# Kernel tuning notes

Measured on AMD Instinct MI355X. Metric: run time of the kernel, lower is better.

## Reference

```python
import jax, jax.numpy as jnp
import numpy as np

N_NODES = 50000
N_EDGES = 300000
N_GRAPHS = 2048
N_FEATS = 128
DIM_OUT = 32


def setup_inputs() -> dict:
    key = jax.random.key(0)
    ks = jax.random.split(key, 10)
    def glorot(k, shape):
        fan_in, fan_out = shape
        lim = (6.0 / (fan_in + fan_out)) ** 0.5
        return jax.random.uniform(k, shape, jnp.float32, -lim, lim)
    x = jax.random.normal(ks[0], (N_NODES, N_FEATS), jnp.float32)
    edge_index = jax.random.randint(ks[1], (2, N_EDGES), 0, N_NODES, jnp.int64)
    batch = jnp.sort(jax.random.randint(ks[2], (N_NODES,), 0, N_GRAPHS, jnp.int64))
    return {
        "x": x,
        "edge_index": edge_index,
        "batch": batch,
        "W1": glorot(ks[3], (N_FEATS, 256)), "b1": jnp.zeros((256,), jnp.float32),
        "W2": glorot(ks[4], (256, 256)),     "b2": jnp.zeros((256,), jnp.float32),
        "W3": glorot(ks[5], (256, 256)),     "b3": jnp.zeros((256,), jnp.float32),
        "Wf1": glorot(ks[6], (256, 128)),    "bf1": jnp.zeros((128,), jnp.float32),
        "Wf2": glorot(ks[7], (128, DIM_OUT)), "bf2": jnp.zeros((DIM_OUT,), jnp.float32),
    }


def _gcn_norm(edge_index, num_nodes):
    # PyG GCNConv default: add self-loops, symmetric D^-1/2 (A+I) D^-1/2 norm.
    loop = jnp.arange(num_nodes, dtype=edge_index.dtype)
    src = jnp.concatenate([edge_index[0], loop])
    dst = jnp.concatenate([edge_index[1], loop])
    deg = jax.ops.segment_sum(jnp.ones_like(dst, jnp.float32), dst, num_segments=num_nodes)
    dinv = jnp.where(deg > 0, deg ** -0.5, 0.0)
    norm = dinv[src] * dinv[dst]  # [E + N]
    return src, dst, norm


def _gcn_conv(x, src, dst, norm, W, b):
    h = x @ W                                # [N, C] transform first (efficient)
    msg = h[src] * norm[:, None]             # gather + scale, [E+N, C]
    agg = jax.ops.segment_sum(msg, dst, num_segments=x.shape[0])
    return agg + b


def reference(x, edge_index, batch, W1, b1, W2, b2, W3, b3, Wf1, bf1, Wf2, bf2):
    n = x.shape[0]
    src, dst, norm = _gcn_norm(edge_index, n)
    h = jax.nn.relu(_gcn_conv(x, src, dst, norm, W1, b1))
    h = jax.nn.relu(_gcn_conv(h, src, dst, norm, W2, b2))
    h = jax.nn.relu(_gcn_conv(h, src, dst, norm, W3, b3))
    # global_mean_pool over batch segment ids
    sums = jax.ops.segment_sum(h, batch, num_segments=N_GRAPHS)
    cnts = jax.ops.segment_sum(jnp.ones((n,), jnp.float32), batch, num_segments=N_GRAPHS)
    hg = sums / jnp.maximum(cnts, 1.0)[:, None]
    h = jax.nn.relu(hg @ Wf1 + bf1)
    return h @ Wf2 + bf2  # [N_GRAPHS, DIM_OUT]
```

## Files before the change

kernel.cpp:

```cpp
#include <hip/hip_runtime.h>
#include <hip/hip_bf16.h>

#define NNODES 50000
#define NEDGES 300000
#define NGRAPH 2048
#define NFEAT  128
#define NHID   256
#define DOUT   32
#define NROWS  50048

typedef __bf16 bf16x8 __attribute__((ext_vector_type(8)));
typedef float  f32x4  __attribute__((ext_vector_type(4)));
typedef unsigned short ushort8v __attribute__((ext_vector_type(8)));
typedef __attribute__((address_space(1))) const void* gas_ptr;
typedef __attribute__((address_space(3))) void* las_ptr;

__device__ __forceinline__ float bf2f(unsigned short u) {
    return __uint_as_float(((unsigned)u) << 16);
}
__device__ __forceinline__ unsigned short f2bf(float f) {
    unsigned u = __float_as_uint(f);
    unsigned r = u + 0x7FFFu + ((u >> 16) & 1u);
    return (unsigned short)(r >> 16);
}

__global__ __launch_bounds__(256) void prep_k(const float* __restrict__ x, unsigned short* __restrict__ x16,
                                              const float* __restrict__ W1, const float* __restrict__ W2,
                                              const float* __restrict__ W3, const float* __restrict__ Wf1,
                                              const float* __restrict__ Wf2,
                                              unsigned short* __restrict__ Wt1, unsigned short* __restrict__ Wt2,
                                              unsigned short* __restrict__ Wt3, unsigned short* __restrict__ Wf1t,
                                              unsigned short* __restrict__ Wf2t,
                                              int* __restrict__ cnt, int* __restrict__ fill) {
    int idx = blockIdx.x * 256 + threadIdx.x;
    if (idx < 800000) {
        int i = idx * 8;
        float4 a = *(const float4*)&x[i];
        float4 b = *(const float4*)&x[i + 4];
        ushort4 lo = { f2bf(a.x), f2bf(a.y), f2bf(a.z), f2bf(a.w) };
        ushort4 hi = { f2bf(b.x), f2bf(b.y), f2bf(b.z), f2bf(b.w) };
        *(ushort4*)&x16[i] = lo;
        *(ushort4*)&x16[i + 4] = hi;
        return;
    }
    int t = idx - 800000;
    if (t < 200704) {
        const float* W; unsigned short* Wt; int K, N, base; bool sw;
        if      (t <  32768) { W = W1;  Wt = Wt1;  K = 128; N = 256; base = 0;      sw = true; }
        else if (t <  98304) { W = W2;  Wt = Wt2;  K = 256; N = 256; base = 32768;  sw = true; }
        else if (t < 163840) { W = W3;  Wt = Wt3;  K = 256; N = 256; base = 98304;  sw = true; }
        else if (t < 196608) { W = Wf1; Wt = Wf1t; K = 256; N = 128; base = 163840; sw = false; }
        else                 { W = Wf2; Wt = Wf2t; K = 128; N = 32;  base = 196608; sw = false; }
        int i = t - base; int n = i / K, k = i - n * K;
        unsigned short v = f2bf(W[(size_t)k * N + n]);
        if (sw) Wt[(k >> 5) * 8192 + n * 32 + (k & 31)] = v;
        else    Wt[i] = v;
        return;
    }
    t -= 200704;
    if (t < NNODES) { cnt[t] = 0; fill[t] = 0; }
}

__global__ __launch_bounds__(256) void edge_hist_k(const int* __restrict__ dst, int* cnt, int E) {
    int e = blockIdx.x * 256 + threadIdx.x;
    if (e < E) atomicAdd(&cnt[dst[e]], 1);
}

__global__ __launch_bounds__(1024) void scan_block_k(const int* __restrict__ cnt, int* __restrict__ rowp,
                                                     int* __restrict__ part, float* __restrict__ dinv, int n) {
    __shared__ int s[1024];
    int tid = threadIdx.x;
    int i = blockIdx.x * 1024 + tid;
    int v = (i < n) ? cnt[i] : 0;
    if (i < n) dinv[i] = rsqrtf((float)(v + 1));
    s[tid] = v;
    __syncthreads();
    for (int off = 1; off < 1024; off <<= 1) {
        int t = (tid >= off) ? s[tid - off] : 0;
        __syncthreads();
        s[tid] += t;
        __syncthreads();
    }
    if (i < n) rowp[i] = s[tid] - v;
    if (tid == 1023) part[blockIdx.x] = s[1023];
}

__global__ __launch_bounds__(256) void scatter_k(const int* __restrict__ src, const int* __restrict__ dst,
                                                 const int* __restrict__ rowp_pre, const int* __restrict__ part,
                                                 int* fill, const float* __restrict__ dinv,
                                                 int* __restrict__ col, float* __restrict__ nrm,
                                                 int* __restrict__ rowp_fin,
                                                 const int* __restrict__ batch, int* __restrict__ gstart,
                                                 int E, int n, int nb) {
    __shared__ int s[64];
    int tid = threadIdx.x;
    if (tid < 64) s[tid] = (tid < nb) ? part[tid] : 0;
    __syncthreads();
    for (int off = 1; off < 64; off <<= 1) {
        int t = 0;
        if (tid < 64 && tid >= off) t = s[tid - off];
        __syncthreads();
        if (tid < 64) s[tid] += t;
        __syncthreads();
    }
    int gid = blockIdx.x * 256 + tid;
    if (gid <= n) {
        if (gid < n) {
            int ch = gid >> 10;
            int base = (ch == 0) ? 0 : s[ch - 1];
            rowp_fin[gid] = rowp_pre[gid] + base;
        } else {
            rowp_fin[n] = s[nb - 1];
        }
    }
    if (gid < n) {
        int b = batch[gid];
        int prev = (gid == 0) ? -1 : batch[gid - 1];
        for (int g = prev + 1; g <= b; ++g) gstart[g] = gid;
        if (gid == n - 1)
            for (int g = b + 1; g <= NGRAPH; ++g) gstart[g] = n;
    }
    if (gid < E) {
        int ss = src[gid], d = dst[gid];
        int ch = d >> 10;
        int base = (ch == 0) ? 0 : s[ch - 1];
        int p = rowp_pre[d] + base + atomicAdd(&fill[d], 1);
        col[p] = ss;
        nrm[p] = dinv[ss] * dinv[d];
    }
}

template<int K>
__global__ __launch_bounds__(512, 2) void gemm_rs_k(const unsigned short* __restrict__ A,
                                                    const unsigned short* __restrict__ Bsw,
                                                    const float* __restrict__ bias,
                                                    unsigned short* __restrict__ C,
                                                    int M, int flags, int ntiles) {
    __shared__ unsigned short tile[2][64 * 264];
    const int tid = threadIdx.x;
    const int lane = tid & 63;
    const int wave = tid >> 6;
    const int m = lane & 15, q = lane >> 4;
    const int wr = (wave >> 2) * 32;
    const int wc = (wave & 3) * 64;

    bf16x8 breg[K / 32][4];
#pragma unroll
    for (int kt = 0; kt < K / 32; ++kt)
#pragma unroll
        for (int j = 0; j < 4; ++j)
            breg[kt][j] = *(const bf16x8*)&Bsw[kt * 8192 + (wc + j * 16 + m) * 32 + q * 8];

    int buf = 0;
    for (int t = blockIdx.x; t < ntiles; t += gridDim.x) {
        const int rowBase = t * 64;
        f32x4 acc[2][4] = {};
#pragma unroll
        for (int kt = 0; kt < K / 32; ++kt) {
            bf16x8 af[2];
#pragma unroll
            for (int i = 0; i < 2; ++i)
                af[i] = *(const bf16x8*)&A[(size_t)(rowBase + wr + i * 16 + m) * K + kt * 32 + q * 8];
#pragma unroll
            for (int i = 0; i < 2; ++i)
#pragma unroll
                for (int j = 0; j < 4; ++j)
                    acc[i][j] = __builtin_amdgcn_mfma_f32_16x16x32_bf16(af[i], breg[kt][j], acc[i][j], 0, 0, 0);
        }
        unsigned short* tb = tile[buf];
#pragma unroll
        for (int i = 0; i < 2; ++i) {
#pragma unroll
            for (int j = 0; j < 4; ++j) {
                int c = wc + j * 16 + m;
                float bv = (flags & 2) ? bias[c] : 0.f;
#pragma unroll
                for (int r = 0; r < 4; ++r) {
                    float v = acc[i][j][r] + bv;
                    if (flags & 1) v = fmaxf(v, 0.f);
                    tb[(wr + i * 16 + q * 4 + r) * 264 + c] = f2bf(v);
                }
            }
        }
        __syncthreads();
#pragma unroll
        for (int u0 = 0; u0 < 4; ++u0) {
            int u = u0 * 512 + tid;
            int row = u >> 5, cc = (u & 31) * 8;
            int rr = rowBase + row;
            if (rr < M)
                *(ushort8v*)&C[(size_t)rr * 256 + cc] = *(const ushort8v*)&tile[buf][row * 264 + cc];
        }
        buf ^= 1;
    }
}

__global__ __launch_bounds__(256) void agg128_k(const unsigned short* __restrict__ x,
                                                const int* __restrict__ rowp, const int* __restrict__ col,
                                                const float* __restrict__ nrm, const float* __restrict__ dinv,
                                                unsigned short* __restrict__ z, int n) {
    int wave = threadIdx.x >> 6;
    int lane = threadIdx.x & 63;
    int st = lane >> 4;
    int li = lane & 15;
    int node = blockIdx.x * 4 + wave;
    if (node >= n) return;
    const ushort8v* tp = (const ushort8v*)x;
    float di = dinv[node], sw = di * di;
    float hsw = (st == 0) ? sw : 0.f;
    ushort8v u = tp[(size_t)node * 16 + li];
    float ac[8];
#pragma unroll
    for (int k = 0; k < 8; ++k) ac[k] = bf2f(u[k]) * hsw;
    int e0 = rowp[node], e1 = rowp[node + 1];
    for (int e = e0 + st; e < e1; e += 8) {
        int c[2]; float w[2];
#pragma unroll
        for (int j = 0; j < 2; ++j) {
            int ee = e + 4 * j;
            bool v = ee < e1;
            c[j] = v ? col[ee] : 0;
            w[j] = v ? nrm[ee] : 0.f;
        }
        ushort8v mm[2];
#pragma unroll
        for (int j = 0; j < 2; ++j) mm[j] = tp[(size_t)c[j] * 16 + li];
#pragma unroll
        for (int j = 0; j < 2; ++j)
#pragma unroll
            for (int k = 0; k < 8; ++k)
                ac[k] += bf2f(mm[j][k]) * w[j];
    }
#pragma unroll
    for (int k = 0; k < 8; ++k) ac[k] += __shfl_down(ac[k], 32, 64);
#pragma unroll
    for (int k = 0; k < 8; ++k) ac[k] += __shfl_down(ac[k], 16, 64);
    if (st == 0) {
        ushort8v o;
#pragma unroll
        for (int k = 0; k < 8; ++k) o[k] = f2bf(ac[k]);
        ((ushort8v*)(z + (size_t)node * 128))[li] = o;
    }
}

__global__ __launch_bounds__(256) void agg256_k(const unsigned short* __restrict__ t,
                                                const int* __restrict__ rowp, const int* __restrict__ col,
                                                const float* __restrict__ nrm, const float* __restrict__ dinv,
                                                unsigned short* __restrict__ z, int n) {
    int wave = threadIdx.x >> 6;
    int lane = threadIdx.x & 63;
    int half = lane >> 5;
    int li   = lane & 31;
    int node = blockIdx.x * 4 + wave;
    if (node >= n) return;
    const ushort8v* tp = (const ushort8v*)t;
    float di = dinv[node], sw = di * di;
    float hsw = half ? 0.f : sw;
    ushort8v u = tp[(size_t)node * 32 + li];
    float ac[8];
#pragma unroll
    for (int k = 0; k < 8; ++k) ac[k] = bf2f(u[k]) * hsw;
    int e0 = rowp[node], e1 = rowp[node + 1];
    for (int e = e0 + half; e < e1; e += 8) {
        int c[4]; float w[4];
#pragma unroll
        for (int j = 0; j < 4; ++j) {
            int ee = e + 2 * j;
            bool v = ee < e1;
            c[j] = v ? col[ee] : 0;
            w[j] = v ? nrm[ee] : 0.f;
        }
        ushort8v mm[4];
#pragma unroll
        for (int j = 0; j < 4; ++j) mm[j] = tp[(size_t)c[j] * 32 + li];
#pragma unroll
        for (int j = 0; j < 4; ++j)
#pragma unroll
            for (int k = 0; k < 8; ++k)
                ac[k] += bf2f(mm[j][k]) * w[j];
    }
#pragma unroll
    for (int k = 0; k < 8; ++k) ac[k] += __shfl_down(ac[k], 32, 64);
    if (half == 0) {
        ushort8v o;
#pragma unroll
        for (int k = 0; k < 8; ++k) o[k] = f2bf(ac[k]);
        ((ushort8v*)(z + (size_t)node * NHID))[li] = o;
    }
}

__global__ __launch_bounds__(256) void pool_k(const unsigned short* __restrict__ h,
                                              const int* __restrict__ gstart,
                                              unsigned short* __restrict__ hg) {
    __shared__ float red[4][256];
    int g = blockIdx.x;
    int wave = threadIdx.x >> 6, lane = threadIdx.x & 63;
    int s = gstart[g], e = gstart[g + 1];
    const ushort4* hp = (const ushort4*)h;
    float4 acc = make_float4(0.f, 0.f, 0.f, 0.f);
    for (int i = s + wave; i < e; i += 4) {
        ushort4 v = hp[(size_t)i * 64 + lane];
        acc.x += bf2f(v.x); acc.y += bf2f(v.y); acc.z += bf2f(v.z); acc.w += bf2f(v.w);
    }
    *(float4*)&red[wave][lane * 4] = acc;
    __syncthreads();
    if (wave == 0) {
        float inv = 1.f / fmaxf((float)(e - s), 1.f);
        float v0 = red[0][lane*4+0] + red[1][lane*4+0] + red[2][lane*4+0] + red[3][lane*4+0];
        float v1 = red[0][lane*4+1] + red[1][lane*4+1] + red[2][lane*4+1] + red[3][lane*4+1];
        float v2 = red[0][lane*4+2] + red[1][lane*4+2] + red[2][lane*4+2] + red[3][lane*4+2];
        float v3 = red[0][lane*4+3] + red[1][lane*4+3] + red[2][lane*4+3] + red[3][lane*4+3];
        ushort4 o = { f2bf(v0 * inv), f2bf(v1 * inv), f2bf(v2 * inv), f2bf(v3 * inv) };
        ((ushort4*)(hg + (size_t)g * NHID))[lane] = o;
    }
}

__global__ __launch_bounds__(256) void mlp_head_k(const unsigned short* __restrict__ HG,
                                                  const unsigned short* __restrict__ Wf1t,
                                                  const unsigned short* __restrict__ Wf2t,
                                                  const float* __restrict__ bf1, const float* __restrict__ bf2,
                                                  float* __restrict__ out) {
    __shared__ unsigned short As1[128 * 32];
    __shared__ unsigned short Bs1[128 * 32];
    __shared__ unsigned short R[128 * 128];
    __shared__ unsigned short Bs2[32 * 128];
    const int tid = threadIdx.x;
    const int lane = tid & 63, wave = tid >> 6;
    const int m = lane & 15, q = lane >> 4;
    const int rowBase = blockIdx.x * 128;
    const int wr = (wave >> 1) * 64;
    const int wc = (wave & 1) * 64;

#pragma unroll
    for (int c2 = 0; c2 < 2; ++c2) {
        const unsigned short* g = &Wf2t[(c2 * 256 + tid) * 8];
        __builtin_amdgcn_global_load_lds((gas_ptr)g, (las_ptr)&Bs2[(c2 * 256 + wave * 64) * 8], 16, 0, 0);
    }

    f32x4 acc[4][4] = {};
    for (int kt = 0; kt < 256; kt += 32) {
#pragma unroll
        for (int c2 = 0; c2 < 2; ++c2) {
            int u = c2 * 256 + tid;
            int row = u >> 2, kp = u & 3;
            const unsigned short* ga = &HG[(size_t)(rowBase + row) * 256 + kt + kp * 8];
            const unsigned short* gb = &Wf1t[(size_t)row * 256 + kt + kp * 8];
            __builtin_amdgcn_global_load_lds((gas_ptr)ga, (las_ptr)&As1[(c2 * 256 + wave * 64) * 8], 16, 0, 0);
            __builtin_amdgcn_global_load_lds((gas_ptr)gb, (las_ptr)&Bs1[(c2 * 256 + wave * 64) * 8], 16, 0, 0);
        }
        __syncthreads();
        bf16x8 af[4], bfr[4];
#pragma unroll
        for (int i = 0; i < 4; ++i) af[i] = *(const bf16x8*)&As1[(wr + i * 16 + m) * 32 + q * 8];
#pragma unroll
        for (int j = 0; j < 4; ++j) bfr[j] = *(const bf16x8*)&Bs1[(wc + j * 16 + m) * 32 + q * 8];
#pragma unroll
        for (int i = 0; i < 4; ++i)
#pragma unroll
            for (int j = 0; j < 4; ++j)
                acc[i][j] = __builtin_amdgcn_mfma_f32_16x16x32_bf16(af[i], bfr[j], acc[i][j], 0, 0, 0);
        __syncthreads();
    }
#pragma unroll
    for (int i = 0; i < 4; ++i)
#pragma unroll
        for (int j = 0; j < 4; ++j) {
            int c = wc + j * 16 + m;
            float bv = bf1[c];
#pragma unroll
            for (int r = 0; r < 4; ++r) {
                int rr = wr + i * 16 + q * 4 + r;
                R[rr * 128 + c] = f2bf(fmaxf(acc[i][j][r] + bv, 0.f));
            }
        }
    __syncthreads();

    const int wr2 = wave * 32;
    f32x4 acc2[2][2] = {};
#pragma unroll
    for (int s2 = 0; s2 < 4; ++s2) {
        bf16x8 af2[2], bf22[2];
#pragma unroll
        for (int i = 0; i < 2; ++i) af2[i] = *(const bf16x8*)&R[(wr2 + i * 16 + m) * 128 + s2 * 32 + q * 8];
#pragma unroll
        for (int ct = 0; ct < 2; ++ct) bf22[ct] = *(const bf16x8*)&Bs2[(ct * 16 + m) * 128 + s2 * 32 + q * 8];
#pragma unroll
        for (int i = 0; i < 2; ++i)
#pragma unroll
            for (int ct = 0; ct < 2; ++ct)
                acc2[i][ct] = __builtin_amdgcn_mfma_f32_16x16x32_bf16(af2[i], bf22[ct], acc2[i][ct], 0, 0, 0);
    }
#pragma unroll
    for (int i = 0; i < 2; ++i)
#pragma unroll
        for (int ct = 0; ct < 2; ++ct) {
            int c = ct * 16 + m;
            float bv = bf2[c];
#pragma unroll
            for (int r = 0; r < 4; ++r) {
                int rr = rowBase + wr2 + i * 16 + q * 4 + r;
                out[(size_t)rr * 32 + c] = acc2[i][ct][r] + bv;
            }
        }
}

extern "C" void kernel_launch(void* const* d_in, const int* in_sizes, int n_in,
                              void* d_out, int out_size, void* d_ws, size_t ws_size,
                              hipStream_t stream) {
    const float* x    = (const float*)d_in[0];
    const int*   ei   = (const int*)d_in[1];
    const int*   batch= (const int*)d_in[2];
    const float* W1   = (const float*)d_in[3];
    const float* b1   = (const float*)d_in[4];
    const float* W2   = (const float*)d_in[5];
    const float* b2   = (const float*)d_in[6];
    const float* W3   = (const float*)d_in[7];
    const float* b3   = (const float*)d_in[8];
    const float* Wf1  = (const float*)d_in[9];
    const float* bf1  = (const float*)d_in[10];
    const float* Wf2  = (const float*)d_in[11];
    const float* bf2  = (const float*)d_in[12];
    float* out = (float*)d_out;

    const int* e_src = ei;
    const int* e_dst = ei + NEDGES;

    char* ws = (char*)d_ws;
    size_t off = 0;
    auto alloc = [&](size_t bytes) -> void* {
        void* p = (void*)(ws + off);
        off += (bytes + 255) & ~(size_t)255;
        return p;
    };
    unsigned short* X16 = (unsigned short*)alloc((size_t)NROWS * NFEAT * 2);
    unsigned short* Za  = (unsigned short*)alloc((size_t)NROWS * NFEAT * 2);
    unsigned short* Ha  = (unsigned short*)alloc((size_t)NROWS * NHID * 2);
    unsigned short* Zb  = (unsigned short*)alloc((size_t)NROWS * NHID * 2);
    unsigned short* Wt1 = (unsigned short*)alloc((size_t)NHID * NFEAT * 2);
    unsigned short* Wt2 = (unsigned short*)alloc((size_t)NHID * NHID * 2);
    unsigned short* Wt3 = (unsigned short*)alloc((size_t)NHID * NHID * 2);
    unsigned short* Wf1t= (unsigned short*)alloc((size_t)NFEAT * NHID * 2);
    unsigned short* Wf2t= (unsigned short*)alloc((size_t)DOUT * NFEAT * 2);
    unsigned short* HG  = (unsigned short*)alloc((size_t)NGRAPH * NHID * 2);
    float* dinv = (float*)alloc((size_t)NNODES * 4);
    int*   cnt  = (int*)alloc((size_t)NNODES * 4);
    int*   fill = (int*)alloc((size_t)NNODES * 4);
    int*   rowp = (int*)alloc((size_t)(NNODES + 1) * 4);
    int*   rowf = (int*)alloc((size_t)(NNODES + 1) * 4);
    int*   col  = (int*)alloc((size_t)NEDGES * 4);
    float* nrm  = (float*)alloc((size_t)NEDGES * 4);
    int*   part = (int*)alloc((size_t)64 * 4);
    int*   gstart = (int*)alloc((size_t)(NGRAPH + 1) * 4);
    (void)alloc(131072);

    const int nb = (NNODES + 1023) / 1024;

    hipLaunchKernelGGL(prep_k, dim3((1050704 + 255) / 256), dim3(256), 0, stream,
                       x, X16, W1, W2, W3, Wf1, Wf2, Wt1, Wt2, Wt3, Wf1t, Wf2t, cnt, fill);
    hipLaunchKernelGGL(edge_hist_k, dim3((NEDGES + 255) / 256), dim3(256), 0, stream, e_dst, cnt, NEDGES);
    hipLaunchKernelGGL(scan_block_k, dim3(nb), dim3(1024), 0, stream, cnt, rowp, part, dinv, NNODES);
    hipLaunchKernelGGL(scatter_k, dim3((NEDGES + 255) / 256), dim3(256), 0, stream,
                       e_src, e_dst, rowp, part, fill, dinv, col, nrm, rowf, batch, gstart,
                       NEDGES, NNODES, nb);

    const int ntiles = NROWS / 64;
    const int nagg  = (NNODES + 3) / 4;
    hipLaunchKernelGGL(agg128_k, dim3(nagg), dim3(256), 0, stream,
                       X16, rowf, col, nrm, dinv, Za, NNODES);
    hipLaunchKernelGGL((gemm_rs_k<128>), dim3(512), dim3(512), 0, stream,
                       Za, Wt1, b1, Ha, NNODES, 3, ntiles);
    hipLaunchKernelGGL(agg256_k, dim3(nagg), dim3(256), 0, stream,
                       Ha, rowf, col, nrm, dinv, Zb, NNODES);
    hipLaunchKernelGGL((gemm_rs_k<256>), dim3(256), dim3(512), 0, stream,
                       Zb, Wt2, b2, Ha, NNODES, 3, ntiles);
    hipLaunchKernelGGL(agg256_k, dim3(nagg), dim3(256), 0, stream,
                       Ha, rowf, col, nrm, dinv, Zb, NNODES);
    hipLaunchKernelGGL((gemm_rs_k<256>), dim3(256), dim3(512), 0, stream,
                       Zb, Wt3, b3, Ha, NNODES, 3, ntiles);

    hipLaunchKernelGGL(pool_k, dim3(NGRAPH), dim3(256), 0, stream, Ha, gstart, HG);

    hipLaunchKernelGGL(mlp_head_k, dim3(NGRAPH / 128), dim3(256), 0, stream,
                       HG, Wf1t, Wf2t, bf1, bf2, out);
}
```

Measured before the change: 301.6 us.

## Fuse neighbor aggregation into GEMM tiles and pack edge column/norm pairs

Replaces the separate aggregation kernels and row-streaming GEMMs with one fused kernel per layer. Each block gathers and normalizes the neighbor features for its 64-row tile straight into an XOR-swizzled LDS tile, then runs MFMA against register-resident weights. This removes the write and re-read of the aggregated intermediate and drops three launches. Edge column indices and norms are also packed into a single int2 array so each edge needs one load. The cost is lower occupancy during the latency-bound gather phase, because the large LDS footprint limits each CU to two blocks, and the gather and MFMA phases now run one after the other inside each block.

```diff
diff --git a/kernel.cpp b/kernel.cpp
--- a/kernel.cpp
+++ b/kernel.cpp
@@ -88,7 +88,7 @@
 __global__ __launch_bounds__(256) void scatter_k(const int* __restrict__ src, const int* __restrict__ dst,
                                                  const int* __restrict__ rowp_pre, const int* __restrict__ part,
                                                  int* fill, const float* __restrict__ dinv,
-                                                 int* __restrict__ col, float* __restrict__ nrm,
+                                                 int2* __restrict__ adj,
                                                  int* __restrict__ rowp_fin,
                                                  const int* __restrict__ batch, int* __restrict__ gstart,
                                                  int E, int n, int nb) {
@@ -125,24 +125,34 @@
         int ch = d >> 10;
         int base = (ch == 0) ? 0 : s[ch - 1];
         int p = rowp_pre[d] + base + atomicAdd(&fill[d], 1);
-        col[p] = ss;
-        nrm[p] = dinv[ss] * dinv[d];
+        int2 a; a.x = ss; a.y = __float_as_int(dinv[ss] * dinv[d]);
+        adj[p] = a;
     }
 }
 
 template<int K>
-__global__ __launch_bounds__(512, 2) void gemm_rs_k(const unsigned short* __restrict__ A,
-                                                    const unsigned short* __restrict__ Bsw,
-                                                    const float* __restrict__ bias,
-                                                    unsigned short* __restrict__ C,
-                                                    int M, int flags, int ntiles) {
-    __shared__ unsigned short tile[2][64 * 264];
+__global__ __launch_bounds__(512, 2) void fused_agg_gemm_k(
+        const unsigned short* __restrict__ T,
+        const int2* __restrict__ adj,
+        const int* __restrict__ rowp,
+        const float* __restrict__ dinv,
+        const unsigned short* __restrict__ Bsw,
+        const float* __restrict__ bias,
+        unsigned short* __restrict__ C,
+        int M, int flags, int ntiles) {
+    constexpr int CH = K / 8;
+    constexpr int NS = 512 / CH;
+    constexpr int RPS = 64 / NS;
+    __shared__ unsigned short At[64 * K];
+    __shared__ unsigned short Et[64 * 264];
     const int tid = threadIdx.x;
     const int lane = tid & 63;
     const int wave = tid >> 6;
     const int m = lane & 15, q = lane >> 4;
     const int wr = (wave >> 2) * 32;
     const int wc = (wave & 3) * 64;
+    const int st = tid / CH;
+    const int li = tid % CH;
 
     bf16x8 breg[K / 32][4];
 #pragma unroll
@@ -151,23 +161,66 @@
         for (int j = 0; j < 4; ++j)
             breg[kt][j] = *(const bf16x8*)&Bsw[kt * 8192 + (wc + j * 16 + m) * 32 + q * 8];
 
-    int buf = 0;
+    char* Atb = (char*)At;
+    const ushort8v* tp = (const ushort8v*)T;
+
     for (int t = blockIdx.x; t < ntiles; t += gridDim.x) {
         const int rowBase = t * 64;
+#pragma unroll
+        for (int s = 0; s < RPS; ++s) {
+            int lr = st * RPS + s;
+            int nd = rowBase + lr;
+            float ac[8] = {0.f, 0.f, 0.f, 0.f, 0.f, 0.f, 0.f, 0.f};
+            if (nd < NNODES) {
+                float di = dinv[nd], sw = di * di;
+                ushort8v u = tp[(size_t)nd * CH + li];
+#pragma unroll
+                for (int k = 0; k < 8; ++k) ac[k] = bf2f(u[k]) * sw;
+                int e0 = rowp[nd], e1 = rowp[nd + 1];
+                for (int e = e0; e < e1; e += 8) {
+                    int c[8]; float w[8];
+#pragma unroll
+                    for (int j = 0; j < 8; ++j) {
+                        int ee = e + j;
+                        bool v = ee < e1;
+                        int2 a = v ? adj[ee] : make_int2(0, 0);
+                        c[j] = a.x; w[j] = __int_as_float(a.y);
+                    }
+                    ushort8v mm[8];
+#pragma unroll
+                    for (int j = 0; j < 8; ++j) mm[j] = tp[(size_t)c[j] * CH + li];
+#pragma unroll
+                    for (int j = 0; j < 8; ++j)
+#pragma unroll
+                        for (int k = 0; k < 8; ++k)
+                            ac[k] += bf2f(mm[j][k]) * w[j];
+                }
+            }
+            ushort8v o;
+#pragma unroll
+            for (int k = 0; k < 8; ++k) o[k] = f2bf(ac[k]);
+            int byteo = (lr * (K * 2) + li * 16) ^ ((lr & 7) << 4);
+            *(ushort8v*)(Atb + byteo) = o;
+        }
+        __syncthreads();
+
         f32x4 acc[2][4] = {};
 #pragma unroll
         for (int kt = 0; kt < K / 32; ++kt) {
             bf16x8 af[2];
 #pragma unroll
-            for (int i = 0; i < 2; ++i)
-                af[i] = *(const bf16x8*)&A[(size_t)(rowBase + wr + i * 16 + m) * K + kt * 32 + q * 8];
+            for (int i = 0; i < 2; ++i) {
+                int lr = wr + i * 16 + m;
+                int byteo = (lr * (K * 2) + kt * 64 + q * 16) ^ ((lr & 7) << 4);
+                af[i] = *(const bf16x8*)(Atb + byteo);
+            }
 #pragma unroll
             for (int i = 0; i < 2; ++i)
 #pragma unroll
                 for (int j = 0; j < 4; ++j)
                     acc[i][j] = __builtin_amdgcn_mfma_f32_16x16x32_bf16(af[i], breg[kt][j], acc[i][j], 0, 0, 0);
         }
-        unsigned short* tb = tile[buf];
+
 #pragma unroll
         for (int i = 0; i < 2; ++i) {
 #pragma unroll
@@ -178,7 +231,7 @@
                 for (int r = 0; r < 4; ++r) {
                     float v = acc[i][j][r] + bv;
                     if (flags & 1) v = fmaxf(v, 0.f);
-                    tb[(wr + i * 16 + q * 4 + r) * 264 + c] = f2bf(v);
+                    Et[(wr + i * 16 + q * 4 + r) * 264 + c] = f2bf(v);
                 }
             }
         }
@@ -189,103 +242,8 @@
             int row = u >> 5, cc = (u & 31) * 8;
             int rr = rowBase + row;
             if (rr < M)
-                *(ushort8v*)&C[(size_t)rr * 256 + cc] = *(const ushort8v*)&tile[buf][row * 264 + cc];
-        }
-        buf ^= 1;
-    }
-}
-
-__global__ __launch_bounds__(256) void agg128_k(const unsigned short* __restrict__ x,
-                                                const int* __restrict__ rowp, const int* __restrict__ col,
-                                                const float* __restrict__ nrm, const float* __restrict__ dinv,
-                                                unsigned short* __restrict__ z, int n) {
-    int wave = threadIdx.x >> 6;
-    int lane = threadIdx.x & 63;
-    int st = lane >> 4;
-    int li = lane & 15;
-    int node = blockIdx.x * 4 + wave;
-    if (node >= n) return;
-    const ushort8v* tp = (const ushort8v*)x;
-    float di = dinv[node], sw = di * di;
-    float hsw = (st == 0) ? sw : 0.f;
-    ushort8v u = tp[(size_t)node * 16 + li];
-    float ac[8];
-#pragma unroll
-    for (int k = 0; k < 8; ++k) ac[k] = bf2f(u[k]) * hsw;
-    int e0 = rowp[node], e1 = rowp[node + 1];
-    for (int e = e0 + st; e < e1; e += 8) {
-        int c[2]; float w[2];
-#pragma unroll
-        for (int j = 0; j < 2; ++j) {
-            int ee = e + 4 * j;
-            bool v = ee < e1;
-            c[j] = v ? col[ee] : 0;
-            w[j] = v ? nrm[ee] : 0.f;
-        }
-        ushort8v mm[2];
-#pragma unroll
-        for (int j = 0; j < 2; ++j) mm[j] = tp[(size_t)c[j] * 16 + li];
-#pragma unroll
-        for (int j = 0; j < 2; ++j)
-#pragma unroll
-            for (int k = 0; k < 8; ++k)
-                ac[k] += bf2f(mm[j][k]) * w[j];
-    }
-#pragma unroll
-    for (int k = 0; k < 8; ++k) ac[k] += __shfl_down(ac[k], 32, 64);
-#pragma unroll
-    for (int k = 0; k < 8; ++k) ac[k] += __shfl_down(ac[k], 16, 64);
-    if (st == 0) {
-        ushort8v o;
-#pragma unroll
-        for (int k = 0; k < 8; ++k) o[k] = f2bf(ac[k]);
-        ((ushort8v*)(z + (size_t)node * 128))[li] = o;
-    }
-}
-
-__global__ __launch_bounds__(256) void agg256_k(const unsigned short* __restrict__ t,
-                                                const int* __restrict__ rowp, const int* __restrict__ col,
-                                                const float* __restrict__ nrm, const float* __restrict__ dinv,
-                                                unsigned short* __restrict__ z, int n) {
-    int wave = threadIdx.x >> 6;
-    int lane = threadIdx.x & 63;
-    int half = lane >> 5;
-    int li   = lane & 31;
-    int node = blockIdx.x * 4 + wave;
-    if (node >= n) return;
-    const ushort8v* tp = (const ushort8v*)t;
-    float di = dinv[node], sw = di * di;
-    float hsw = half ? 0.f : sw;
-    ushort8v u = tp[(size_t)node * 32 + li];
-    float ac[8];
-#pragma unroll
-    for (int k = 0; k < 8; ++k) ac[k] = bf2f(u[k]) * hsw;
-    int e0 = rowp[node], e1 = rowp[node + 1];
-    for (int e = e0 + half; e < e1; e += 8) {
-        int c[4]; float w[4];
-#pragma unroll
-        for (int j = 0; j < 4; ++j) {
-            int ee = e + 2 * j;
-            bool v = ee < e1;
-            c[j] = v ? col[ee] : 0;
-            w[j] = v ? nrm[ee] : 0.f;
-        }
-        ushort8v mm[4];
-#pragma unroll
-        for (int j = 0; j < 4; ++j) mm[j] = tp[(size_t)c[j] * 32 + li];
-#pragma unroll
-        for (int j = 0; j < 4; ++j)
-#pragma unroll
-            for (int k = 0; k < 8; ++k)
-                ac[k] += bf2f(mm[j][k]) * w[j];
-    }
-#pragma unroll
-    for (int k = 0; k < 8; ++k) ac[k] += __shfl_down(ac[k], 32, 64);
-    if (half == 0) {
-        ushort8v o;
-#pragma unroll
-        for (int k = 0; k < 8; ++k) o[k] = f2bf(ac[k]);
-        ((ushort8v*)(z + (size_t)node * NHID))[li] = o;
+                *(ushort8v*)&C[(size_t)rr * 256 + cc] = *(const ushort8v*)&Et[row * 264 + cc];
+        }
     }
 }
 
@@ -433,9 +391,8 @@
         return p;
     };
     unsigned short* X16 = (unsigned short*)alloc((size_t)NROWS * NFEAT * 2);
-    unsigned short* Za  = (unsigned short*)alloc((size_t)NROWS * NFEAT * 2);
     unsigned short* Ha  = (unsigned short*)alloc((size_t)NROWS * NHID * 2);
-    unsigned short* Zb  = (unsigned short*)alloc((size_t)NROWS * NHID * 2);
+    unsigned short* Hb  = (unsigned short*)alloc((size_t)NROWS * NHID * 2);
     unsigned short* Wt1 = (unsigned short*)alloc((size_t)NHID * NFEAT * 2);
     unsigned short* Wt2 = (unsigned short*)alloc((size_t)NHID * NHID * 2);
     unsigned short* Wt3 = (unsigned short*)alloc((size_t)NHID * NHID * 2);
@@ -447,8 +404,7 @@
     int*   fill = (int*)alloc((size_t)NNODES * 4);
     int*   rowp = (int*)alloc((size_t)(NNODES + 1) * 4);
     int*   rowf = (int*)alloc((size_t)(NNODES + 1) * 4);
-    int*   col  = (int*)alloc((size_t)NEDGES * 4);
-    float* nrm  = (float*)alloc((size_t)NEDGES * 4);
+    int2*  adj  = (int2*)alloc((size_t)NEDGES * 8);
     int*   part = (int*)alloc((size_t)64 * 4);
     int*   gstart = (int*)alloc((size_t)(NGRAPH + 1) * 4);
     (void)alloc(131072);
@@ -460,23 +416,16 @@
     hipLaunchKernelGGL(edge_hist_k, dim3((NEDGES + 255) / 256), dim3(256), 0, stream, e_dst, cnt, NEDGES);
     hipLaunchKernelGGL(scan_block_k, dim3(nb), dim3(1024), 0, stream, cnt, rowp, part, dinv, NNODES);
     hipLaunchKernelGGL(scatter_k, dim3((NEDGES + 255) / 256), dim3(256), 0, stream,
-                       e_src, e_dst, rowp, part, fill, dinv, col, nrm, rowf, batch, gstart,
+                       e_src, e_dst, rowp, part, fill, dinv, adj, rowf, batch, gstart,
                        NEDGES, NNODES, nb);
 
     const int ntiles = NROWS / 64;
-    const int nagg  = (NNODES + 3) / 4;
-    hipLaunchKernelGGL(agg128_k, dim3(nagg), dim3(256), 0, stream,
-                       X16, rowf, col, nrm, dinv, Za, NNODES);
-    hipLaunchKernelGGL((gemm_rs_k<128>), dim3(512), dim3(512), 0, stream,
-                       Za, Wt1, b1, Ha, NNODES, 3, ntiles);
-    hipLaunchKernelGGL(agg256_k, dim3(nagg), dim3(256), 0, stream,
-                       Ha, rowf, col, nrm, dinv, Zb, NNODES);
-    hipLaunchKernelGGL((gemm_rs_k<256>), dim3(256), dim3(512), 0, stream,
-                       Zb, Wt2, b2, Ha, NNODES, 3, ntiles);
-    hipLaunchKernelGGL(agg256_k, dim3(nagg), dim3(256), 0, stream,
-                       Ha, rowf, col, nrm, dinv, Zb, NNODES);
-    hipLaunchKernelGGL((gemm_rs_k<256>), dim3(256), dim3(512), 0, stream,
-                       Zb, Wt3, b3, Ha, NNODES, 3, ntiles);
+    hipLaunchKernelGGL((fused_agg_gemm_k<128>), dim3(512), dim3(512), 0, stream,
+                       X16, adj, rowf, dinv, Wt1, b1, Ha, NNODES, 3, ntiles);
+    hipLaunchKernelGGL((fused_agg_gemm_k<256>), dim3(512), dim3(512), 0, stream,
+                       Ha, adj, rowf, dinv, Wt2, b2, Hb, NNODES, 3, ntiles);
+    hipLaunchKernelGGL((fused_agg_gemm_k<256>), dim3(512), dim3(512), 0, stream,
+                       Hb, adj, rowf, dinv, Wt3, b3, Ha, NNODES, 3, ntiles);
 
     hipLaunchKernelGGL(pool_k, dim3(NGRAPH), dim3(256), 0, stream, Ha, gstart, HG);
 
```

After: 340.7 us. 13.0% more time.
